# Optimization experiments

Measured on AMD Instinct MI355X. Metric: run time of the kernel, lower is better.

The kernel has to match this reference:

```python
import jax, jax.numpy as jnp
import numpy as np

B = 16
L = 1024  # signal_length


def setup_inputs() -> dict:
    key = jax.random.key(0)
    ks = jax.random.split(key, 6)
    X = jax.random.normal(ks[0], (B, L), dtype=jnp.float32)
    # encoder projection Fc (the repo initializes it uniform(-0.5, 0.5))
    Fc = (jax.random.uniform(ks[1], (L, 2 * L), dtype=jnp.float32) - 0.5)
    # MLP weights (kaiming-ish scaling kept small for numerical sanity)
    W1 = jax.random.normal(ks[2], (2 * L, 50 * L), dtype=jnp.float32) * 0.02
    b1 = jax.random.normal(ks[3], (50 * L,), dtype=jnp.float32) * 0.02
    W2 = jax.random.normal(ks[4], (50 * L, 2 * L), dtype=jnp.float32) * 0.02
    b2 = jax.random.normal(ks[5], (2 * L,), dtype=jnp.float32) * 0.02
    return {"X": X, "Fc": Fc, "W1": W1, "b1": b1, "W2": W2, "b2": b2}


def _decode(z):
    # z: [B, 2L] -> reconstructed signal [B, L]
    yr = z[:, :L]
    yi = z[:, L:]
    amp = jnp.sqrt(yr * yr + yi * yi) / L          # [B, L]
    ph = jnp.arctan2(yi, yr)                        # [B, L]
    t = jnp.arange(L, dtype=jnp.float32)
    arg = (2.0 * jnp.pi / L) * (t[:, None] * t[None, :])  # [L(t), L(f)]
    # sinusoids[b, t, f] = amp[b, f] * cos(arg[t, f] + ph[b, f]); reduce over f
    sinusoids = amp[:, None, :] * jnp.cos(arg[None, :, :] + ph[:, None, :])
    return jnp.sum(sinusoids, axis=-1)              # [B, L]


def reference(X, Fc, W1, b1, W2, b2):
    y_pred = X @ Fc                                  # encoder: [B, 2L]
    h = jax.nn.sigmoid(y_pred @ W1 + b1)             # [B, 50L]
    z = h @ W2 + b2                                  # [B, 2L]
    return _decode(z)                                # [B, L]
```

## Files before the change

kernel.cpp:

```cpp
#include <hip/hip_runtime.h>
#include <math.h>

#define LL    1024
#define BB    16
#define NN1   2048
#define NNH   51200

using f32x2 = __attribute__((ext_vector_type(2))) float;

__global__ void k_xt(const float* __restrict__ X, float* __restrict__ XT,
                     const float* __restrict__ b2, float* __restrict__ z2) {
    int id = blockIdx.x * 256 + threadIdx.x;
    if (id < LL * BB) {
        int n = id >> 4, b = id & 15;
        XT[id] = X[b * LL + n];
    } else {
        int j = id - LL * BB;
        z2[j] = b2[j & (NN1 - 1)];
    }
}

template <int CH, int NCOL>
__global__ __launch_bounds__(256, 4) void k_gpart(
        const float* __restrict__ AT,
        const float* __restrict__ W,
        float* __restrict__ part) {
    const int t  = threadIdx.x;
    const int n2 = blockIdx.x * 512 + t * 2;
    const int s  = blockIdx.y;
    const int m0 = s * CH;

    float2 acc[BB];
#pragma unroll
    for (int r = 0; r < BB; ++r) acc[r] = make_float2(0.f, 0.f);

    const float* wp = W  + (size_t)m0 * NCOL + n2;
    const float* ap = AT + (size_t)m0 * BB;
#pragma unroll 8
    for (int m = 0; m < CH; ++m) {
        const f32x2 w = __builtin_nontemporal_load((const f32x2*)wp);
        wp += NCOL;
        const float4 a0 = *(const float4*)(ap + 0);
        const float4 a1 = *(const float4*)(ap + 4);
        const float4 a2 = *(const float4*)(ap + 8);
        const float4 a3 = *(const float4*)(ap + 12);
        ap += BB;
        acc[ 0].x = fmaf(a0.x, w.x, acc[ 0].x);  acc[ 0].y = fmaf(a0.x, w.y, acc[ 0].y);
        acc[ 1].x = fmaf(a0.y, w.x, acc[ 1].x);  acc[ 1].y = fmaf(a0.y, w.y, acc[ 1].y);
        acc[ 2].x = fmaf(a0.z, w.x, acc[ 2].x);  acc[ 2].y = fmaf(a0.z, w.y, acc[ 2].y);
        acc[ 3].x = fmaf(a0.w, w.x, acc[ 3].x);  acc[ 3].y = fmaf(a0.w, w.y, acc[ 3].y);
        acc[ 4].x = fmaf(a1.x, w.x, acc[ 4].x);  acc[ 4].y = fmaf(a1.x, w.y, acc[ 4].y);
        acc[ 5].x = fmaf(a1.y, w.x, acc[ 5].x);  acc[ 5].y = fmaf(a1.y, w.y, acc[ 5].y);
        acc[ 6].x = fmaf(a1.z, w.x, acc[ 6].x);  acc[ 6].y = fmaf(a1.z, w.y, acc[ 6].y);
        acc[ 7].x = fmaf(a1.w, w.x, acc[ 7].x);  acc[ 7].y = fmaf(a1.w, w.y, acc[ 7].y);
        acc[ 8].x = fmaf(a2.x, w.x, acc[ 8].x);  acc[ 8].y = fmaf(a2.x, w.y, acc[ 8].y);
        acc[ 9].x = fmaf(a2.y, w.x, acc[ 9].x);  acc[ 9].y = fmaf(a2.y, w.y, acc[ 9].y);
        acc[10].x = fmaf(a2.z, w.x, acc[10].x);  acc[10].y = fmaf(a2.z, w.y, acc[10].y);
        acc[11].x = fmaf(a2.w, w.x, acc[11].x);  acc[11].y = fmaf(a2.w, w.y, acc[11].y);
        acc[12].x = fmaf(a3.x, w.x, acc[12].x);  acc[12].y = fmaf(a3.x, w.y, acc[12].y);
        acc[13].x = fmaf(a3.y, w.x, acc[13].x);  acc[13].y = fmaf(a3.y, w.y, acc[13].y);
        acc[14].x = fmaf(a3.z, w.x, acc[14].x);  acc[14].y = fmaf(a3.z, w.y, acc[14].y);
        acc[15].x = fmaf(a3.w, w.x, acc[15].x);  acc[15].y = fmaf(a3.w, w.y, acc[15].y);
    }

    float* pp = part + ((size_t)s * BB) * NCOL + n2;
#pragma unroll
    for (int r = 0; r < BB; ++r)
        *(float2*)(pp + (size_t)r * NCOL) = acc[r];
}

template <bool SIG>
__global__ __launch_bounds__(256) void k_redT(
        const float* __restrict__ part,
        const float* __restrict__ bias,
        float* __restrict__ outT,
        int N, int splits) {
    const int n  = blockIdx.x * 256 + threadIdx.x;
    const int b0 = blockIdx.y * 4;
    float acc[4] = {0.f, 0.f, 0.f, 0.f};
    for (int s = 0; s < splits; ++s) {
        const float* p = part + ((size_t)s * BB + b0) * N + n;
#pragma unroll
        for (int j = 0; j < 4; ++j) acc[j] += p[(size_t)j * N];
    }
    const float bv = bias ? bias[n] : 0.f;
#pragma unroll
    for (int j = 0; j < 4; ++j) {
        float v = acc[j] + bv;
        if (SIG) v = 1.f / (1.f + __expf(-v));
        acc[j] = v;
    }
    *(float4*)(outT + (size_t)n * BB + b0) = make_float4(acc[0], acc[1], acc[2], acc[3]);
}

__global__ __launch_bounds__(256) void k_redN(
        const float* __restrict__ part,
        float* __restrict__ z2) {
    const int id = blockIdx.x * 256 + threadIdx.x;
    const int s0 = blockIdx.y * 64;
    float acc0 = 0.f, acc1 = 0.f;
    for (int s = 0; s < 64; s += 2) {
        acc0 += part[(size_t)(s0 + s)     * (BB * NN1) + id];
        acc1 += part[(size_t)(s0 + s + 1) * (BB * NN1) + id];
    }
    atomicAdd(&z2[id], acc0 + acc1);
}

__global__ __launch_bounds__(256) void k_decode(const float* __restrict__ z2,
                                                float* __restrict__ out) {
    __shared__ float yr[LL], yi[LL];
    __shared__ float partial[3 * 64];
    const int t  = threadIdx.x;
    const int b  = blockIdx.y;
    const int il = t & 63;
    const int i  = blockIdx.x * 64 + il;
    const int jq = t >> 6;
    for (int j = t; j < LL; j += 256) {
        yr[j] = z2[b * NN1 + j];
        yi[j] = z2[b * NN1 + LL + j];
    }
    __syncthreads();
    const int j0 = jq * 256;
    float acc = 0.f;
    int r = (j0 * i) & (LL - 1);
    for (int jj = 0; jj < 256; ++jj) {
        float rev = (float)r * (1.0f / LL);
        float c = __builtin_amdgcn_cosf(rev);
        float s = __builtin_amdgcn_sinf(rev);
        acc = fmaf(yr[j0 + jj], c, acc);
        acc = fmaf(-yi[j0 + jj], s, acc);
        r = (r + i) & (LL - 1);
    }
    if (jq > 0) partial[(jq - 1) * 64 + il] = acc;
    __syncthreads();
    if (jq == 0)
        out[b * LL + i] = (acc + partial[il] + partial[64 + il] + partial[128 + il])
                          * (1.0f / LL);
}

extern "C" void kernel_launch(void* const* d_in, const int* in_sizes, int n_in,
                              void* d_out, int out_size, void* d_ws, size_t ws_size,
                              hipStream_t stream) {
    const float* X  = (const float*)d_in[0];
    const float* Fc = (const float*)d_in[1];
    const float* W1 = (const float*)d_in[2];
    const float* b1 = (const float*)d_in[3];
    const float* W2 = (const float*)d_in[4];
    const float* b2 = (const float*)d_in[5];
    float* out = (float*)d_out;

    float* ws     = (float*)d_ws;
    float* XT     = ws;
    float* ypredT = XT     + LL * BB;
    float* hT     = ypredT + NN1 * BB;
    float* z2     = hT     + NNH * BB;
    float* parts0 = z2     + BB * NN1;
    float* parts1 = parts0 + 32 * BB * NN1;
    float* parts2 = parts1 + 8 * BB * NNH;

    k_xt<<<dim3((LL * BB + BB * NN1) / 256), 256, 0, stream>>>(X, XT, b2, z2);
    k_gpart<32, NN1><<<dim3(NN1 / 512, 32), 256, 0, stream>>>(XT, Fc, parts0);
    k_redT<false><<<dim3(NN1 / 256, 4), 256, 0, stream>>>(parts0, nullptr, ypredT, NN1, 32);
    k_gpart<256, NNH><<<dim3(NNH / 512, 8), 256, 0, stream>>>(ypredT, W1, parts1);
    k_redT<true><<<dim3(NNH / 256, 4), 256, 0, stream>>>(parts1, b1, hT, NNH, 8);
    k_gpart<200, NN1><<<dim3(NN1 / 512, 256), 256, 0, stream>>>(hT, W2, parts2);
    k_redN<<<dim3(BB * NN1 / 256, 4), 256, 0, stream>>>(parts2, z2);
    k_decode<<<dim3(LL / 64, BB), 256, 0, stream>>>(z2, out);
}
```

Measured before the change: 213.3 us.

## Fuse X transpose into first GEMM, fold bias init into reduction, halve split-K

```diff
diff --git a/kernel.cpp b/kernel.cpp
--- a/kernel.cpp
+++ b/kernel.cpp
@@ -8,16 +8,41 @@
 
 using f32x2 = __attribute__((ext_vector_type(2))) float;
 
-__global__ void k_xt(const float* __restrict__ X, float* __restrict__ XT,
-                     const float* __restrict__ b2, float* __restrict__ z2) {
-    int id = blockIdx.x * 256 + threadIdx.x;
-    if (id < LL * BB) {
-        int n = id >> 4, b = id & 15;
-        XT[id] = X[b * LL + n];
-    } else {
-        int j = id - LL * BB;
-        z2[j] = b2[j & (NN1 - 1)];
-    }
+template <int CH>
+__global__ __launch_bounds__(256, 4) void k_g0(
+        const float* __restrict__ X,
+        const float* __restrict__ Fc,
+        float* __restrict__ part) {
+    const int t  = threadIdx.x;
+    const int n2 = blockIdx.x * 512 + t * 2;
+    const int s  = blockIdx.y;
+    const int m0 = s * CH;
+
+    float2 acc[BB];
+#pragma unroll
+    for (int r = 0; r < BB; ++r) acc[r] = make_float2(0.f, 0.f);
+
+    const float* wp = Fc + (size_t)m0 * NN1 + n2;
+    const float* xp = X + m0;
+#pragma unroll 4
+    for (int m = 0; m < CH; ++m) {
+        const f32x2 w = __builtin_nontemporal_load((const f32x2*)wp);
+        wp += NN1;
+        float a[BB];
+#pragma unroll
+        for (int b = 0; b < BB; ++b) a[b] = xp[b * LL];
+        xp += 1;
+#pragma unroll
+        for (int b = 0; b < BB; ++b) {
+            acc[b].x = fmaf(a[b], w.x, acc[b].x);
+            acc[b].y = fmaf(a[b], w.y, acc[b].y);
+        }
+    }
+
+    float* pp = part + ((size_t)s * BB) * NN1 + n2;
+#pragma unroll
+    for (int r = 0; r < BB; ++r)
+        *(float2*)(pp + (size_t)r * NN1) = acc[r];
 }
 
 template <int CH, int NCOL>
@@ -93,13 +118,31 @@
     *(float4*)(outT + (size_t)n * BB + b0) = make_float4(acc[0], acc[1], acc[2], acc[3]);
 }
 
+__global__ __launch_bounds__(256) void k_redT0z(
+        const float* __restrict__ part,
+        float* __restrict__ outT,
+        const float* __restrict__ b2, float* __restrict__ z2) {
+    const int flat = (blockIdx.y * 8 + blockIdx.x) * 256 + threadIdx.x;
+    *(float4*)(z2 + flat * 4) = *(const float4*)(b2 + ((flat * 4) & (NN1 - 1)));
+
+    const int n  = blockIdx.x * 256 + threadIdx.x;
+    const int b0 = blockIdx.y * 4;
+    float acc[4] = {0.f, 0.f, 0.f, 0.f};
+    for (int s = 0; s < 32; ++s) {
+        const float* p = part + ((size_t)s * BB + b0) * NN1 + n;
+#pragma unroll
+        for (int j = 0; j < 4; ++j) acc[j] += p[(size_t)j * NN1];
+    }
+    *(float4*)(outT + (size_t)n * BB + b0) = make_float4(acc[0], acc[1], acc[2], acc[3]);
+}
+
 __global__ __launch_bounds__(256) void k_redN(
         const float* __restrict__ part,
         float* __restrict__ z2) {
     const int id = blockIdx.x * 256 + threadIdx.x;
-    const int s0 = blockIdx.y * 64;
+    const int s0 = blockIdx.y * 32;
     float acc0 = 0.f, acc1 = 0.f;
-    for (int s = 0; s < 64; s += 2) {
+    for (int s = 0; s < 32; s += 2) {
         acc0 += part[(size_t)(s0 + s)     * (BB * NN1) + id];
         acc1 += part[(size_t)(s0 + s + 1) * (BB * NN1) + id];
     }
@@ -150,20 +193,18 @@
     float* out = (float*)d_out;
 
     float* ws     = (float*)d_ws;
-    float* XT     = ws;
-    float* ypredT = XT     + LL * BB;
+    float* ypredT = ws;
     float* hT     = ypredT + NN1 * BB;
     float* z2     = hT     + NNH * BB;
     float* parts0 = z2     + BB * NN1;
     float* parts1 = parts0 + 32 * BB * NN1;
-    float* parts2 = parts1 + 8 * BB * NNH;
-
-    k_xt<<<dim3((LL * BB + BB * NN1) / 256), 256, 0, stream>>>(X, XT, b2, z2);
-    k_gpart<32, NN1><<<dim3(NN1 / 512, 32), 256, 0, stream>>>(XT, Fc, parts0);
-    k_redT<false><<<dim3(NN1 / 256, 4), 256, 0, stream>>>(parts0, nullptr, ypredT, NN1, 32);
-    k_gpart<256, NNH><<<dim3(NNH / 512, 8), 256, 0, stream>>>(ypredT, W1, parts1);
-    k_redT<true><<<dim3(NNH / 256, 4), 256, 0, stream>>>(parts1, b1, hT, NNH, 8);
-    k_gpart<200, NN1><<<dim3(NN1 / 512, 256), 256, 0, stream>>>(hT, W2, parts2);
+    float* parts2 = parts1 + 4 * BB * NNH;
+
+    k_g0<32><<<dim3(NN1 / 512, 32), 256, 0, stream>>>(X, Fc, parts0);
+    k_redT0z<<<dim3(NN1 / 256, 4), 256, 0, stream>>>(parts0, ypredT, b2, z2);
+    k_gpart<512, NNH><<<dim3(NNH / 512, 4), 256, 0, stream>>>(ypredT, W1, parts1);
+    k_redT<true><<<dim3(NNH / 256, 4), 256, 0, stream>>>(parts1, b1, hT, NNH, 4);
+    k_gpart<400, NN1><<<dim3(NN1 / 512, 128), 256, 0, stream>>>(hT, W2, parts2);
     k_redN<<<dim3(BB * NN1 / 256, 4), 256, 0, stream>>>(parts2, z2);
     k_decode<<<dim3(LL / 64, BB), 256, 0, stream>>>(z2, out);
 }
```

Measured after the change: 253.9 us. 19.0% more time.
